# Kernel optimization log

Measured on AMD Instinct MI355X. Metric: run time of the kernel, lower is better.

Reference implementation:

```python
import jax, jax.numpy as jnp
import numpy as np

H = 12
D_MODEL = 768
D_K = D_MODEL // H  # 64


def setup_inputs() -> dict:
    key = jax.random.key(0)
    ks = jax.random.split(key, 16)
    B, S, D = 4, 1024, D_MODEL
    scale = 1.0 / np.sqrt(D)
    inp = {
        "query": jax.random.normal(ks[0], (B, S, D), jnp.float32),
        "key": jax.random.normal(ks[1], (B, S, D), jnp.float32),
        "value": jax.random.normal(ks[2], (B, S, D), jnp.float32),
        "times": jax.random.normal(ks[3], (2, B, S, D), jnp.float32),
        # learned params (Linear weights stored torch-style [out, in])
        "Wq": jax.random.normal(ks[4], (D, D), jnp.float32) * scale,
        "bq": jnp.zeros((D,), jnp.float32),
        "Wk": jax.random.normal(ks[5], (D, D), jnp.float32) * scale,
        "bk": jnp.zeros((D,), jnp.float32),
        "Wv": jax.random.normal(ks[6], (D, D), jnp.float32) * scale,
        "bv": jnp.zeros((D,), jnp.float32),
        "Wt": jax.random.normal(ks[7], (D, D), jnp.float32) * scale,
        "bt": jnp.zeros((D,), jnp.float32),
        "Wo": jax.random.normal(ks[8], (D, D), jnp.float32) * scale,
        "bo": jnp.zeros((D,), jnp.float32),
    }
    return inp


def _split_heads(x, B, S):
    # [B,S,D] -> [B,H,S,D_K]
    return x.reshape(B, S, H, D_K).transpose(0, 2, 1, 3)


def reference(query, key, value, times, Wq, bq, Wk, bk, Wv, bv, Wt, bt, Wo, bo):
    B, S, D = query.shape
    inv_sqrt_dk = 1.0 / jnp.sqrt(jnp.asarray(D_K, query.dtype))
    # q/k/v projections are identical across time-loop iterations; hoist them.
    q = _split_heads(query @ Wq.T + bq, B, S)   # [B,H,S,dk]
    k = _split_heads(key @ Wk.T + bk, B, S)
    v = _split_heads(value @ Wv.T + bv, B, S)
    x = jnp.zeros_like(q)
    n_times = times.shape[0]
    for i in range(n_times):  # small fixed loop over time embeddings
        t = _split_heads(times[i] @ Wt.T + bt, B, S)
        # dual-score attention: query.time + query.key, each scaled by 1/sqrt(d_k)
        scores = (jnp.einsum('bhqd,bhkd->bhqk', q, t)
                  + jnp.einsum('bhqd,bhkd->bhqk', q, k)) * inv_sqrt_dk
        p = jax.nn.softmax(scores, axis=-1)
        x = x + jnp.einsum('bhqk,bhkd->bhqd', p, v)
    x = x.transpose(0, 2, 1, 3).reshape(B, S, H * D_K)
    return x @ Wo.T + bo
```

## Files before the change

kernel.cpp:

```cpp
#include <hip/hip_runtime.h>
#include <hip/hip_fp16.h>

typedef _Float16 v8h __attribute__((ext_vector_type(8)));
typedef _Float16 v4h __attribute__((ext_vector_type(4)));
typedef _Float16 v2h __attribute__((ext_vector_type(2)));
typedef float v4f __attribute__((ext_vector_type(4)));

#define MFMA_F16 __builtin_amdgcn_mfma_f32_16x16x32_f16
#define EXP2F __builtin_amdgcn_exp2f
#define SCHED_FENCE() __builtin_amdgcn_sched_barrier(0)

__device__ static inline v2h pkrtz(float a, float b) {
  return __builtin_bit_cast(v2h, __builtin_amdgcn_cvt_pkrtz(a, b));
}

__device__ static inline void async_copy16(const void* g, void* l) {
  __builtin_amdgcn_global_load_lds(
      (const __attribute__((address_space(1))) void*)g,
      (__attribute__((address_space(3))) void*)l, 16, 0, 0);
}

struct CastArgs {
  const float* src[5];
  _Float16* dst[5];
  int start[6];
  float scale[5];
};
__global__ void cast_all(CastArgs a) {
  const int g = blockIdx.x * 256 + threadIdx.x;
  if (g >= a.start[5]) return;
  int z = 0;
  #pragma unroll
  for (int i = 1; i < 5; ++i) if (g >= a.start[i]) z = i;
  const int i0 = g - a.start[z];
  const float sc = a.scale[z];
  const float* s = a.src[z] + (size_t)i0 * 8;
  const float4 f0 = *(const float4*)s;
  const float4 f1 = *(const float4*)(s + 4);
  v8h o = {(_Float16)(f0.x * sc), (_Float16)(f0.y * sc),
           (_Float16)(f0.z * sc), (_Float16)(f0.w * sc),
           (_Float16)(f1.x * sc), (_Float16)(f1.y * sc),
           (_Float16)(f1.z * sc), (_Float16)(f1.w * sc)};
  *(v8h*)(a.dst[z] + (size_t)i0 * 8) = o;
}

struct ProjArgs {
  const float* A[5];
  const _Float16* W[5];
  const float* b[5];
  void* out[5];
  float bscale[5];
  int mode[5];
};

__global__ __launch_bounds__(256) void gemm_proj(ProjArgs g) {
  __shared__ float a_lds[128 * 64];
  __shared__ _Float16 w_lds[128 * 64];
  const int tid = threadIdx.x;
  const int w = tid >> 6, lane = tid & 63, quad = lane >> 4, l16 = lane & 15;

  const int hw = blockIdx.x + blockIdx.y * 6 + blockIdx.z * 192;
  const int o = (hw & 7) * 120 + (hw >> 3);
  const int n0 = (o % 6) * 128;
  const int m0 = ((o / 6) & 31) * 128;
  const int z = o / 192;

  const float* A = g.A[z];
  const _Float16* W = g.W[z];
  const int wm = (w >> 1) * 64, wn = (w & 1) * 64;

  size_t srcOffW[4]; int ldsOffW[4];
  #pragma unroll
  for (int i = 0; i < 4; ++i) {
    const int c = i * 256 + tid, row = c >> 3, slot = c & 7;
    srcOffW[i] = (size_t)row * 768 + (size_t)((slot ^ (row & 7)) * 8);
    ldsOffW[i] = c * 8;
  }
  size_t srcOffA[8]; int ldsOffA[8];
  #pragma unroll
  for (int i = 0; i < 8; ++i) {
    const int c = i * 256 + tid, row = c >> 4, hp = c & 15;
    const int hl = hp ^ (row & 15);
    srcOffA[i] = (size_t)row * 768 + (size_t)(hl * 4);
    ldsOffA[i] = c * 4;
  }

  auto stage = [&](int kc) {
    #pragma unroll
    for (int i = 0; i < 8; ++i)
      async_copy16(A + (size_t)m0 * 768 + kc + srcOffA[i], &a_lds[ldsOffA[i]]);
    #pragma unroll
    for (int i = 0; i < 4; ++i)
      async_copy16(W + (size_t)n0 * 768 + kc + srcOffW[i], &w_lds[ldsOffW[i]]);
  };

  int adrA[4][2][2];
  #pragma unroll
  for (int mt = 0; mt < 4; ++mt)
    #pragma unroll
    for (int kh = 0; kh < 2; ++kh)
      #pragma unroll
      for (int hf = 0; hf < 2; ++hf) {
        const int r = wm + mt * 16 + l16, sl = kh * 4 + quad;
        adrA[mt][kh][hf] = r * 256 + (((sl * 2 + hf) ^ (r & 15)) * 16);
      }

  v4f acc[4][4] = {};

  for (int k = 0; k < 12; ++k) {
    __syncthreads();
    stage(k * 64);
    __syncthreads();
    const char* aL = (const char*)a_lds;
    #pragma unroll
    for (int kh = 0; kh < 2; ++kh) {
      v8h af[4], bf[4];
      #pragma unroll
      for (int mt = 0; mt < 4; ++mt) {
        const v4f fa0 = *(const v4f*)(aL + adrA[mt][kh][0]);
        const v4f fa1 = *(const v4f*)(aL + adrA[mt][kh][1]);
        const v2h p0 = pkrtz(fa0[0], fa0[1]), p1 = pkrtz(fa0[2], fa0[3]);
        const v2h p2 = pkrtz(fa1[0], fa1[1]), p3 = pkrtz(fa1[2], fa1[3]);
        af[mt] = v8h{p0[0], p0[1], p1[0], p1[1], p2[0], p2[1], p3[0], p3[1]};
      }
      #pragma unroll
      for (int nt = 0; nt < 4; ++nt) {
        const int r = wn + nt * 16 + l16;
        bf[nt] = *(const v8h*)&w_lds[r * 64 + (((kh * 4 + quad) ^ (r & 7)) * 8)];
      }
      __builtin_amdgcn_s_setprio(1);
      #pragma unroll
      for (int mt = 0; mt < 4; ++mt)
        #pragma unroll
        for (int nt = 0; nt < 4; ++nt)
          acc[mt][nt] = MFMA_F16(af[mt], bf[nt], acc[mt][nt], 0, 0, 0);
      __builtin_amdgcn_s_setprio(0);
    }
  }

  const int mode = g.mode[z];
  #pragma unroll
  for (int nt = 0; nt < 4; ++nt) {
    const int col = n0 + wn + nt * 16 + l16;
    const float bv = g.b[z][col] * g.bscale[z];
    if (mode == 1) {
      _Float16* outp = (_Float16*)g.out[z];
      const int h = col >> 6, dk = col & 63;
      #pragma unroll
      for (int mt = 0; mt < 4; ++mt) {
        const int row = m0 + wm + mt * 16 + quad * 4;
        const int b = row >> 10, s = row & 1023;
        const int sp = (s & ~31) | ((s & 12) << 1) | ((s & 16) >> 2);
        v4h pack = {(_Float16)(acc[mt][nt][0] + bv), (_Float16)(acc[mt][nt][1] + bv),
                    (_Float16)(acc[mt][nt][2] + bv), (_Float16)(acc[mt][nt][3] + bv)};
        *(v4h*)&outp[(size_t)((b * 12 + h) * 64 + dk) * 1024 + sp] = pack;
      }
    } else {
      _Float16* outp = (_Float16*)g.out[z];
      #pragma unroll
      for (int mt = 0; mt < 4; ++mt)
        #pragma unroll
        for (int r = 0; r < 4; ++r) {
          const int row = m0 + wm + mt * 16 + quad * 4 + r;
          outp[(size_t)row * 768 + col] = (_Float16)(acc[mt][nt][r] + bv);
        }
    }
  }
}

struct OutArgs { const _Float16* A; const _Float16* W; const float* b; float* out; };

__global__ __launch_bounds__(256) void gemm_out(OutArgs g) {
  __shared__ _Float16 a_lds[2 * 64 * 64];
  __shared__ _Float16 w_lds[2 * 128 * 64];
  const int tid = threadIdx.x;
  const int w = tid >> 6, lane = tid & 63, quad = lane >> 4, l16 = lane & 15;
  const int m0 = blockIdx.x * 64, n0 = blockIdx.y * 128;
  const int wm = (w >> 1) * 32, wn = (w & 1) * 64;

  size_t srcOffW[4]; int ldsOffW[4];
  #pragma unroll
  for (int i = 0; i < 4; ++i) {
    const int c = i * 256 + tid, row = c >> 3, slot = c & 7;
    srcOffW[i] = (size_t)row * 768 + (size_t)((slot ^ (row & 7)) * 8);
    ldsOffW[i] = (i * 256 + w * 64) * 8;
  }
  auto stage = [&](int kc, int buf) {
    #pragma unroll
    for (int i = 0; i < 2; ++i)
      async_copy16(g.A + (size_t)m0 * 768 + kc + srcOffW[i],
                   &a_lds[buf * 4096 + ldsOffW[i]]);
    #pragma unroll
    for (int i = 0; i < 4; ++i)
      async_copy16(g.W + (size_t)n0 * 768 + kc + srcOffW[i],
                   &w_lds[buf * 8192 + ldsOffW[i]]);
  };

  v4f acc[2][4] = {};
  stage(0, 0);

  for (int k0 = 0; k0 < 768; k0 += 64) {
    const int cur = (k0 >> 6) & 1;
    const bool hn = k0 + 64 < 768;
    if (hn) stage(k0 + 64, cur ^ 1);
    SCHED_FENCE();
    if (hn) asm volatile("s_waitcnt vmcnt(6) lgkmcnt(0)" ::: "memory");
    else    asm volatile("s_waitcnt vmcnt(0) lgkmcnt(0)" ::: "memory");
    SCHED_FENCE();
    __builtin_amdgcn_s_barrier();
    SCHED_FENCE();

    const _Float16* al = &a_lds[cur * 4096];
    const _Float16* wl = &w_lds[cur * 8192];
    #pragma unroll
    for (int kh = 0; kh < 2; ++kh) {
      v8h af[2], bf[4];
      #pragma unroll
      for (int mt = 0; mt < 2; ++mt) {
        const int r = wm + mt * 16 + l16;
        af[mt] = *(const v8h*)&al[r * 64 + (((kh * 4 + quad) ^ (r & 7)) * 8)];
      }
      #pragma unroll
      for (int nt = 0; nt < 4; ++nt) {
        const int r = wn + nt * 16 + l16;
        bf[nt] = *(const v8h*)&wl[r * 64 + (((kh * 4 + quad) ^ (r & 7)) * 8)];
      }
      __builtin_amdgcn_s_setprio(1);
      #pragma unroll
      for (int mt = 0; mt < 2; ++mt)
        #pragma unroll
        for (int nt = 0; nt < 4; ++nt)
          acc[mt][nt] = MFMA_F16(af[mt], bf[nt], acc[mt][nt], 0, 0, 0);
      __builtin_amdgcn_s_setprio(0);
    }
    SCHED_FENCE();
    __builtin_amdgcn_s_barrier();
    SCHED_FENCE();
  }

  #pragma unroll
  for (int nt = 0; nt < 4; ++nt) {
    const int col = n0 + wn + nt * 16 + l16;
    const float bv = g.b[col];
    #pragma unroll
    for (int mt = 0; mt < 2; ++mt)
      #pragma unroll
      for (int r = 0; r < 4; ++r) {
        const int row = m0 + wm + mt * 16 + quad * 4 + r;
        g.out[(size_t)row * 768 + col] = acc[mt][nt][r] + bv;
      }
  }
}

__global__ __launch_bounds__(256) void attn(
    const _Float16* __restrict__ Q,
    const _Float16* __restrict__ Kp, const _Float16* __restrict__ T0p,
    const _Float16* __restrict__ T1p,
    const _Float16* __restrict__ Vt,
    _Float16* __restrict__ X)
{
  __shared__ _Float16 lds[6 * 4096];

  const int tid = threadIdx.x;
  const int w = tid >> 6, lane = tid & 63, quad = lane >> 4, l16 = lane & 15;

  const int orig = blockIdx.y * 16 + blockIdx.x;
  const int wgid = (orig & 7) * 96 + (orig >> 3);
  const int bh = wgid >> 4, q0 = (wgid & 15) * 64;
  const int b = bh / 12, h = bh % 12;
  const size_t base = (size_t)b * 1024 * 768 + h * 64;

  const _Float16* ks  = Kp + base;
  const _Float16* t0s = T0p + base;
  const _Float16* t1s = T1p + base;
  const _Float16* vs  = Vt + (size_t)bh * 64 * 1024;

  size_t ktOff[2], vOff[2]; int ldsOff[2];
  #pragma unroll
  for (int i = 0; i < 2; ++i) {
    const int c = i * 256 + w * 64 + lane, row = c >> 3, slot = c & 7;
    const int logical = slot ^ (row & 7);
    ktOff[i] = (size_t)row * 768 + (size_t)(logical * 8);
    vOff[i] = (size_t)row * 1024 + (size_t)(logical * 8);
    ldsOff[i] = c * 8;
  }

  v8h kreg[2], t0reg[2], t1reg[2];
  auto issueLoads = [&](int buf) {
    #pragma unroll
    for (int i = 0; i < 2; ++i) {
      kreg[i]  = *(const v8h*)(ks + ktOff[i]);
      t0reg[i] = *(const v8h*)(t0s + ktOff[i]);
      t1reg[i] = *(const v8h*)(t1s + ktOff[i]);
    }
    #pragma unroll
    for (int i = 0; i < 2; ++i)
      async_copy16(vs + vOff[i], &lds[16384 + buf * 4096 + ldsOff[i]]);
    ks += 64 * 768; t0s += 64 * 768; t1s += 64 * 768; vs += 64;
  };
  auto finishStage = [&](int buf) {
    #pragma unroll
    for (int i = 0; i < 2; ++i) {
      *(v8h*)&lds[buf * 4096 + ldsOff[i]]        = kreg[i] + t0reg[i];
      *(v8h*)&lds[8192 + buf * 4096 + ldsOff[i]] = kreg[i] + t1reg[i];
    }
  };

  const _Float16* Qw = Q + base + (size_t)(q0 + w * 16) * 768;
  const v8h qf0 = *(const v8h*)(Qw + (size_t)l16 * 768 + quad * 8);
  const v8h qf1 = *(const v8h*)(Qw + (size_t)l16 * 768 + 32 + quad * 8);

  int ra0[4], ra1[4];
  #pragma unroll
  for (int t = 0; t < 4; ++t) {
    const int r = t * 16 + l16, rw = r & 7;
    ra0[t] = (r * 64 + ((quad ^ rw) * 8)) * 2;
    ra1[t] = ra0[t] ^ 64;
  }

  const _Float16 one = (_Float16)1.f;
  const v8h ones8 = {one, one, one, one, one, one, one, one};
  v4f o[2][4] = {};
  v4f osum[2] = {};

  issueLoads(0);
  finishStage(0);

  #pragma unroll 2
  for (int cc = 0; cc < 16; ++cc) {
    __syncthreads();
    const int B = (cc & 1) * 8192;
    if (cc < 15) issueLoads((cc + 1) & 1);

    const char* L = (const char*)lds;

    v4f s[2][4];
    __builtin_amdgcn_s_setprio(1);
    #pragma unroll
    for (int kvt = 0; kvt < 4; ++kvt) {
      const v8h k00 = *(const v8h*)(L + B + ra0[kvt]);
      const v8h k01 = *(const v8h*)(L + B + ra1[kvt]);
      const v8h k10 = *(const v8h*)(L + 16384 + B + ra0[kvt]);
      const v8h k11 = *(const v8h*)(L + 16384 + B + ra1[kvt]);
      s[0][kvt] = MFMA_F16(k00, qf0, v4f{}, 0, 0, 0);
      s[0][kvt] = MFMA_F16(k01, qf1, s[0][kvt], 0, 0, 0);
      s[1][kvt] = MFMA_F16(k10, qf0, v4f{}, 0, 0, 0);
      s[1][kvt] = MFMA_F16(k11, qf1, s[1][kvt], 0, 0, 0);
    }
    __builtin_amdgcn_s_setprio(0);

    v8h pb8[2][2];
    #pragma unroll
    for (int t = 0; t < 2; ++t)
      #pragma unroll
      for (int gg = 0; gg < 2; ++gg) {
        const v4f sa = s[t][gg * 2], sb = s[t][gg * 2 + 1];
        const v2h a0 = pkrtz(EXP2F(sa[0]), EXP2F(sa[1]));
        const v2h a1 = pkrtz(EXP2F(sa[2]), EXP2F(sa[3]));
        const v2h b0 = pkrtz(EXP2F(sb[0]), EXP2F(sb[1]));
        const v2h b1 = pkrtz(EXP2F(sb[2]), EXP2F(sb[3]));
        pb8[t][gg] = v8h{a0[0], a0[1], a1[0], a1[1], b0[0], b0[1], b1[0], b1[1]};
        osum[t] = MFMA_F16(ones8, pb8[t][gg], osum[t], 0, 0, 0);
      }

    __builtin_amdgcn_s_setprio(1);
    #pragma unroll
    for (int dkt = 0; dkt < 4; ++dkt) {
      const v8h v0 = *(const v8h*)(L + 32768 + B + ra0[dkt]);
      const v8h v1 = *(const v8h*)(L + 32768 + B + ra1[dkt]);
      o[0][dkt] = MFMA_F16(v0, pb8[0][0], o[0][dkt], 0, 0, 0);
      o[0][dkt] = MFMA_F16(v1, pb8[0][1], o[0][dkt], 0, 0, 0);
      o[1][dkt] = MFMA_F16(v0, pb8[1][0], o[1][dkt], 0, 0, 0);
      o[1][dkt] = MFMA_F16(v1, pb8[1][1], o[1][dkt], 0, 0, 0);
    }
    __builtin_amdgcn_s_setprio(0);

    if (cc < 15) finishStage((cc + 1) & 1);
  }

  const float i0 = 1.0f / osum[0][0], i1 = 1.0f / osum[1][0];

  _Float16* Xw = X + base + (size_t)(q0 + w * 16 + l16) * 768;
  #pragma unroll
  for (int dkt = 0; dkt < 4; ++dkt) {
    v4h pack;
    #pragma unroll
    for (int r = 0; r < 4; ++r)
      pack[r] = (_Float16)(o[0][dkt][r] * i0 + o[1][dkt][r] * i1);
    *(v4h*)&Xw[dkt * 16 + quad * 4] = pack;
  }
}

extern "C" void kernel_launch(void* const* d_in, const int* in_sizes, int n_in,
                              void* d_out, int out_size, void* d_ws, size_t ws_size,
                              hipStream_t stream) {
  const float* query = (const float*)d_in[0];
  const float* key   = (const float*)d_in[1];
  const float* value = (const float*)d_in[2];
  const float* times = (const float*)d_in[3];
  const float* Wq = (const float*)d_in[4];  const float* bq = (const float*)d_in[5];
  const float* Wk = (const float*)d_in[6];  const float* bk = (const float*)d_in[7];
  const float* Wv = (const float*)d_in[8];  const float* bv = (const float*)d_in[9];
  const float* Wt = (const float*)d_in[10]; const float* bt = (const float*)d_in[11];
  const float* Wo = (const float*)d_in[12]; const float* bo = (const float*)d_in[13];
  float* out = (float*)d_out;

  const size_t NELEM = (size_t)4096 * 768;
  const size_t WELEM = (size_t)768 * 768;
  const float QSCALE = 0.125f * 1.4426950408889634f;

  char* ws = (char*)d_ws;
  size_t off = 0;
  auto alloc = [&](size_t bytes) {
    void* p = ws + off; off += (bytes + 255) & ~(size_t)255; return p;
  };
  _Float16* wqh = (_Float16*)alloc(WELEM * 2);
  _Float16* wkh = (_Float16*)alloc(WELEM * 2);
  _Float16* wvh = (_Float16*)alloc(WELEM * 2);
  _Float16* wth = (_Float16*)alloc(WELEM * 2);
  _Float16* woh = (_Float16*)alloc(WELEM * 2);
  _Float16* Qh  = (_Float16*)alloc(NELEM * 2);
  _Float16* Kh  = (_Float16*)alloc(NELEM * 2);
  _Float16* T0h = (_Float16*)alloc(NELEM * 2);
  _Float16* T1h = (_Float16*)alloc(NELEM * 2);
  _Float16* Vt  = (_Float16*)alloc(NELEM * 2);
  _Float16* Xh  = (_Float16*)alloc(NELEM * 2);

  CastArgs ca = {};
  const int nW8 = (int)(WELEM / 8);
  const float* csrc[5] = {Wq, Wk, Wv, Wt, Wo};
  _Float16* cdst[5] = {wqh, wkh, wvh, wth, woh};
  int acc8 = 0;
  for (int i = 0; i < 5; ++i) {
    ca.src[i] = csrc[i]; ca.dst[i] = cdst[i];
    ca.start[i] = acc8;
    acc8 += nW8;
    ca.scale[i] = (i == 0) ? QSCALE : 1.0f;
  }
  ca.start[5] = acc8;
  cast_all<<<dim3((acc8 + 255) / 256), 256, 0, stream>>>(ca);

  ProjArgs pa = {};
  pa.A[0] = key;           pa.W[0] = wkh; pa.b[0] = bk; pa.out[0] = Kh;
  pa.bscale[0] = 1.0f; pa.mode[0] = 0;
  pa.A[1] = times;         pa.W[1] = wth; pa.b[1] = bt; pa.out[1] = T0h;
  pa.bscale[1] = 1.0f; pa.mode[1] = 0;
  pa.A[2] = times + NELEM; pa.W[2] = wth; pa.b[2] = bt; pa.out[2] = T1h;
  pa.bscale[2] = 1.0f; pa.mode[2] = 0;
  pa.A[3] = query;         pa.W[3] = wqh; pa.b[3] = bq; pa.out[3] = Qh;
  pa.bscale[3] = QSCALE; pa.mode[3] = 0;
  pa.A[4] = value;         pa.W[4] = wvh; pa.b[4] = bv; pa.out[4] = Vt;
  pa.bscale[4] = 1.0f; pa.mode[4] = 1;
  gemm_proj<<<dim3(6, 32, 5), 256, 0, stream>>>(pa);

  attn<<<dim3(16, 48), 256, 0, stream>>>(Qh, Kh, T0h, T1h, Vt, Xh);

  OutArgs oa = {Xh, woh, bo, out};
  gemm_out<<<dim3(64, 6), 256, 0, stream>>>(oa);
}
```

Before: 224.9 us.

## Pre-cast activations to fp16 before projection GEMMs and remap grid

Extends the cast kernel to also convert query, key, value and both time slices to fp16, using the output buffer as scratch for the time slices. The projection GEMM then stages fp16 A tiles directly instead of fp32 tiles that were converted in registers. This halves LDS and load traffic in the GEMM and removes the per-fragment conversions. In exchange it adds a separate pass that reads all fp32 activations and writes fp16 copies. It also changes the block-to-tile swizzle to a 2D grid, adds a runtime K bound, and sets unroll 1 on the K loops.

```diff
diff --git a/kernel.cpp b/kernel.cpp
--- a/kernel.cpp
+++ b/kernel.cpp
@@ -21,17 +21,17 @@
 }
 
 struct CastArgs {
-  const float* src[5];
-  _Float16* dst[5];
-  int start[6];
-  float scale[5];
+  const float* src[10];
+  _Float16* dst[10];
+  int start[11];
+  float scale[10];
 };
 __global__ void cast_all(CastArgs a) {
   const int g = blockIdx.x * 256 + threadIdx.x;
-  if (g >= a.start[5]) return;
+  if (g >= a.start[10]) return;
   int z = 0;
   #pragma unroll
-  for (int i = 1; i < 5; ++i) if (g >= a.start[i]) z = i;
+  for (int i = 1; i < 10; ++i) if (g >= a.start[i]) z = i;
   const int i0 = g - a.start[z];
   const float sc = a.scale[z];
   const float* s = a.src[z] + (size_t)i0 * 8;
@@ -45,83 +45,59 @@
 }
 
 struct ProjArgs {
-  const float* A[5];
+  const _Float16* A[5];
   const _Float16* W[5];
   const float* b[5];
   void* out[5];
   float bscale[5];
+  int K[5];
   int mode[5];
 };
 
 __global__ __launch_bounds__(256) void gemm_proj(ProjArgs g) {
-  __shared__ float a_lds[128 * 64];
+  __shared__ _Float16 a_lds[128 * 64];
   __shared__ _Float16 w_lds[128 * 64];
   const int tid = threadIdx.x;
   const int w = tid >> 6, lane = tid & 63, quad = lane >> 4, l16 = lane & 15;
 
-  const int hw = blockIdx.x + blockIdx.y * 6 + blockIdx.z * 192;
-  const int o = (hw & 7) * 120 + (hw >> 3);
-  const int n0 = (o % 6) * 128;
-  const int m0 = ((o / 6) & 31) * 128;
-  const int z = o / 192;
-
-  const float* A = g.A[z];
+  const int z = blockIdx.y;
+  const int bx = blockIdx.x;
+  const int wg = (bx & 7) * 24 + (bx >> 3);
+  const int n0 = (wg % 6) * 128;
+  const int m0 = (wg / 6) * 128;
+
+  const _Float16* A = g.A[z];
   const _Float16* W = g.W[z];
+  const int KK = g.K[z];
   const int wm = (w >> 1) * 64, wn = (w & 1) * 64;
 
-  size_t srcOffW[4]; int ldsOffW[4];
+  size_t srcOff[4]; int ldsOff[4];
   #pragma unroll
   for (int i = 0; i < 4; ++i) {
     const int c = i * 256 + tid, row = c >> 3, slot = c & 7;
-    srcOffW[i] = (size_t)row * 768 + (size_t)((slot ^ (row & 7)) * 8);
-    ldsOffW[i] = c * 8;
-  }
-  size_t srcOffA[8]; int ldsOffA[8];
-  #pragma unroll
-  for (int i = 0; i < 8; ++i) {
-    const int c = i * 256 + tid, row = c >> 4, hp = c & 15;
-    const int hl = hp ^ (row & 15);
-    srcOffA[i] = (size_t)row * 768 + (size_t)(hl * 4);
-    ldsOffA[i] = c * 4;
-  }
-
-  auto stage = [&](int kc) {
-    #pragma unroll
-    for (int i = 0; i < 8; ++i)
-      async_copy16(A + (size_t)m0 * 768 + kc + srcOffA[i], &a_lds[ldsOffA[i]]);
-    #pragma unroll
-    for (int i = 0; i < 4; ++i)
-      async_copy16(W + (size_t)n0 * 768 + kc + srcOffW[i], &w_lds[ldsOffW[i]]);
-  };
-
-  int adrA[4][2][2];
-  #pragma unroll
-  for (int mt = 0; mt < 4; ++mt)
-    #pragma unroll
-    for (int kh = 0; kh < 2; ++kh)
-      #pragma unroll
-      for (int hf = 0; hf < 2; ++hf) {
-        const int r = wm + mt * 16 + l16, sl = kh * 4 + quad;
-        adrA[mt][kh][hf] = r * 256 + (((sl * 2 + hf) ^ (r & 15)) * 16);
-      }
+    srcOff[i] = (size_t)row * 768 + (size_t)((slot ^ (row & 7)) * 8);
+    ldsOff[i] = (i * 256 + w * 64) * 8;
+  }
 
   v4f acc[4][4] = {};
 
-  for (int k = 0; k < 12; ++k) {
+  #pragma unroll 1
+  for (int k0 = 0; k0 < KK; k0 += 64) {
     __syncthreads();
-    stage(k * 64);
+    #pragma unroll
+    for (int i = 0; i < 4; ++i) {
+      async_copy16(A + (size_t)m0 * 768 + k0 + srcOff[i], &a_lds[ldsOff[i]]);
+      async_copy16(W + (size_t)n0 * 768 + k0 + srcOff[i], &w_lds[ldsOff[i]]);
+    }
     __syncthreads();
-    const char* aL = (const char*)a_lds;
+
     #pragma unroll
     for (int kh = 0; kh < 2; ++kh) {
       v8h af[4], bf[4];
       #pragma unroll
       for (int mt = 0; mt < 4; ++mt) {
-        const v4f fa0 = *(const v4f*)(aL + adrA[mt][kh][0]);
-        const v4f fa1 = *(const v4f*)(aL + adrA[mt][kh][1]);
-        const v2h p0 = pkrtz(fa0[0], fa0[1]), p1 = pkrtz(fa0[2], fa0[3]);
-        const v2h p2 = pkrtz(fa1[0], fa1[1]), p3 = pkrtz(fa1[2], fa1[3]);
-        af[mt] = v8h{p0[0], p0[1], p1[0], p1[1], p2[0], p2[1], p3[0], p3[1]};
+        const int r = wm + mt * 16 + l16;
+        af[mt] = *(const v8h*)&a_lds[r * 64 + (((kh * 4 + quad) ^ (r & 7)) * 8)];
       }
       #pragma unroll
       for (int nt = 0; nt < 4; ++nt) {
@@ -199,6 +175,7 @@
   v4f acc[2][4] = {};
   stage(0, 0);
 
+  #pragma unroll 1
   for (int k0 = 0; k0 < 768; k0 += 64) {
     const int cur = (k0 >> 6) & 1;
     const bool hn = k0 + 64 < 768;
@@ -425,33 +402,39 @@
   _Float16* T1h = (_Float16*)alloc(NELEM * 2);
   _Float16* Vt  = (_Float16*)alloc(NELEM * 2);
   _Float16* Xh  = (_Float16*)alloc(NELEM * 2);
+  _Float16* qin = (_Float16*)alloc(NELEM * 2);
+  _Float16* kin = (_Float16*)alloc(NELEM * 2);
+  _Float16* vin = (_Float16*)alloc(NELEM * 2);
+  _Float16* t0in = (_Float16*)d_out;
+  _Float16* t1in = t0in + NELEM;
 
   CastArgs ca = {};
-  const int nW8 = (int)(WELEM / 8);
-  const float* csrc[5] = {Wq, Wk, Wv, Wt, Wo};
-  _Float16* cdst[5] = {wqh, wkh, wvh, wth, woh};
+  const int nA8 = (int)(NELEM / 8), nW8 = (int)(WELEM / 8);
+  const float* csrc[10] = {query, key, value, times, times + NELEM,
+                           Wq, Wk, Wv, Wt, Wo};
+  _Float16* cdst[10] = {qin, kin, vin, t0in, t1in, wqh, wkh, wvh, wth, woh};
   int acc8 = 0;
-  for (int i = 0; i < 5; ++i) {
+  for (int i = 0; i < 10; ++i) {
     ca.src[i] = csrc[i]; ca.dst[i] = cdst[i];
     ca.start[i] = acc8;
-    acc8 += nW8;
-    ca.scale[i] = (i == 0) ? QSCALE : 1.0f;
-  }
-  ca.start[5] = acc8;
+    acc8 += (i < 5) ? nA8 : nW8;
+    ca.scale[i] = (i == 5) ? QSCALE : 1.0f;
+  }
+  ca.start[10] = acc8;
   cast_all<<<dim3((acc8 + 255) / 256), 256, 0, stream>>>(ca);
 
   ProjArgs pa = {};
-  pa.A[0] = key;           pa.W[0] = wkh; pa.b[0] = bk; pa.out[0] = Kh;
-  pa.bscale[0] = 1.0f; pa.mode[0] = 0;
-  pa.A[1] = times;         pa.W[1] = wth; pa.b[1] = bt; pa.out[1] = T0h;
-  pa.bscale[1] = 1.0f; pa.mode[1] = 0;
-  pa.A[2] = times + NELEM; pa.W[2] = wth; pa.b[2] = bt; pa.out[2] = T1h;
-  pa.bscale[2] = 1.0f; pa.mode[2] = 0;
-  pa.A[3] = query;         pa.W[3] = wqh; pa.b[3] = bq; pa.out[3] = Qh;
-  pa.bscale[3] = QSCALE; pa.mode[3] = 0;
-  pa.A[4] = value;         pa.W[4] = wvh; pa.b[4] = bv; pa.out[4] = Vt;
-  pa.bscale[4] = 1.0f; pa.mode[4] = 1;
-  gemm_proj<<<dim3(6, 32, 5), 256, 0, stream>>>(pa);
+  pa.A[0] = kin;  pa.W[0] = wkh; pa.b[0] = bk; pa.out[0] = Kh;
+  pa.bscale[0] = 1.0f; pa.K[0] = 768; pa.mode[0] = 0;
+  pa.A[1] = t0in; pa.W[1] = wth; pa.b[1] = bt; pa.out[1] = T0h;
+  pa.bscale[1] = 1.0f; pa.K[1] = 768; pa.mode[1] = 0;
+  pa.A[2] = t1in; pa.W[2] = wth; pa.b[2] = bt; pa.out[2] = T1h;
+  pa.bscale[2] = 1.0f; pa.K[2] = 768; pa.mode[2] = 0;
+  pa.A[3] = qin;  pa.W[3] = wqh; pa.b[3] = bq; pa.out[3] = Qh;
+  pa.bscale[3] = QSCALE; pa.K[3] = 768; pa.mode[3] = 0;
+  pa.A[4] = vin;  pa.W[4] = wvh; pa.b[4] = bv; pa.out[4] = Vt;
+  pa.bscale[4] = 1.0f; pa.K[4] = 768; pa.mode[4] = 1;
+  gemm_proj<<<dim3(192, 5), 256, 0, stream>>>(pa);
 
   attn<<<dim3(16, 48), 256, 0, stream>>>(Qh, Kh, T0h, T1h, Vt, Xh);
 
```

After: 222.1 us. No clear change (-1.2%).
